# Kernel optimization log

Measured on AMD Instinct MI355X. Metric: run time of the kernel, lower is better.

## Reference

```python
import jax, jax.numpy as jnp
import numpy as np

BITS = 4
N_PACK = 32 // BITS  # int32 compression
GROUPSIZE = 128
MASK = (1 << BITS) - 1


def _unpack_int32(q, axis):
    """Unpack int32 tensor into N_PACK low-bit values along `axis`.
    Element j*N_PACK+e comes from bits [BITS*e, BITS*(e+1)) of packed word j."""
    parts = [ (q >> (BITS * e)) & MASK for e in range(N_PACK) ]
    u = jnp.stack(parts, axis=axis + 1)  # (..., P, N_PACK, ...)
    shape = list(q.shape)
    shape[axis] = shape[axis] * N_PACK
    return u.reshape(shape)


def setup_inputs() -> dict:
    key = jax.random.key(0)
    k1, k2, k3, k4, k5 = jax.random.split(key, 5)
    in_f, out_f = 4096, 12288
    tokens = 8192
    n_groups = in_f // GROUPSIZE  # 32
    x = jax.random.normal(k1, (tokens, in_f), dtype=jnp.float32)
    scales = jax.random.uniform(k2, (n_groups, out_f), dtype=jnp.float32) * 0.01 + 1e-3
    bias = jax.random.normal(k3, (out_f,), dtype=jnp.float32)
    qweight = jax.random.randint(k4, (in_f // N_PACK, out_f), jnp.iinfo(jnp.int32).min, jnp.iinfo(jnp.int32).max, dtype=jnp.int32)
    qzeros = jax.random.randint(k5, (n_groups, out_f // N_PACK), jnp.iinfo(jnp.int32).min, jnp.iinfo(jnp.int32).max, dtype=jnp.int32)
    return {"x": x, "scales": scales, "bias": bias, "qweight": qweight, "qzeros": qzeros}


def reference(x, scales, bias, qweight, qzeros):
    in_f = qweight.shape[0] * N_PACK
    out_f = qweight.shape[1]
    n_groups = scales.shape[0]
    # Unpack 4-bit weights along input-channel axis: (in_f, out_f), values 0..15
    w_int = _unpack_int32(qweight, axis=0).astype(scales.dtype)
    # Unpack zero points along output-channel axis; optimum format stores zp-1
    zp = (_unpack_int32(qzeros, axis=1) + 1).astype(scales.dtype)  # (n_groups, out_f)
    # Per-group dequant: group g covers input channels [g*GROUPSIZE, (g+1)*GROUPSIZE)
    w = (w_int.reshape(n_groups, GROUPSIZE, out_f) - zp[:, None, :]) * scales[:, None, :]
    w = w.reshape(in_f, out_f)
    # Linear: y = x @ W^T with W = w.T, i.e. x @ w
    return x @ w + bias
```

## Files before the change

kernel.cpp:

```cpp
#include <hip/hip_runtime.h>
#include <hip/hip_bf16.h>


typedef __attribute__((ext_vector_type(8))) short short8;
typedef __attribute__((ext_vector_type(4))) float f32x4;
typedef __attribute__((ext_vector_type(16))) float f32x16;

__device__ __forceinline__ short f2bf(float f) {
  unsigned u = __float_as_uint(f);
  u += 0x7fffu + ((u >> 16) & 1u);
  return (short)(u >> 16);
}

__device__ __forceinline__ void gload_lds16(const void* g, void* l) {
  __builtin_amdgcn_global_load_lds(
      (const __attribute__((address_space(1))) void*)g,
      (__attribute__((address_space(3))) void*)l,
      16, 0, 0);
}

__device__ __forceinline__ void bar() {
  asm volatile("" ::: "memory");
  __builtin_amdgcn_s_barrier();
  asm volatile("" ::: "memory");
}
__device__ __forceinline__ void wait_vm8() {
  asm volatile("s_waitcnt vmcnt(8)" ::: "memory");
}
__device__ __forceinline__ void wait_vm4() {
  asm volatile("s_waitcnt vmcnt(4)" ::: "memory");
}
__device__ __forceinline__ void wait_vm0() {
  asm volatile("s_waitcnt vmcnt(0)" ::: "memory");
}

__global__ __launch_bounds__(256) void dequant_tile_kernel(
    const int* __restrict__ qweight, const int* __restrict__ qzeros,
    const float* __restrict__ scales, short* __restrict__ Bt,
    int N, int K) {
  const int kt = K >> 5;
  const int bx = blockIdx.x;
  const int nb = bx / kt, h = bx - nb * kt;
  const int t = threadIdx.x;
  const int n = nb * 256 + t;
  const int g = h >> 2;
  const float sc = scales[(size_t)g * N + n];
  const int zw = qzeros[(size_t)g * (N >> 3) + (n >> 3)];
  const float zs = -(float)(((zw >> ((n & 7) * 4)) & 15) + 1) * sc;
  char* dst = (char*)Bt + (size_t)bx * 16384;
#pragma unroll
  for (int kw = 0; kw < 4; ++kw) {
    const int w = qweight[(size_t)(h * 4 + kw) * N + n];
    short8 v;
#pragma unroll
    for (int e = 0; e < 8; ++e)
      v[e] = f2bf(fmaf((float)((w >> (4 * e)) & 15), sc, zs));
    const int c = ((t >> 5) << 7) + ((kw >> 1) << 6) + ((kw & 1) << 5) + (t & 31);
    *(short8*)(dst + c * 16) = v;
  }
}

__global__ __launch_bounds__(256) void cvt_tile_kernel(
    const float* __restrict__ x, short* __restrict__ xb, int K) {
  const int kt = K >> 5;
  const int bx = blockIdx.x;
  const int mb = bx / kt, h = bx - mb * kt;
  const float* xs = x + (size_t)mb * 256 * K + h * 32;
  char* dst = (char*)xb + (size_t)bx * 16384;
#pragma unroll
  for (int p = 0; p < 4; ++p) {
    const int t2 = p * 256 + threadIdx.x;
    const int row = t2 >> 2, kq = t2 & 3;
    const float* s = xs + (size_t)row * K + kq * 8;
    float4 f0 = *(const float4*)s;
    float4 f1 = *(const float4*)(s + 4);
    short8 v;
    v[0] = f2bf(f0.x); v[1] = f2bf(f0.y); v[2] = f2bf(f0.z); v[3] = f2bf(f0.w);
    v[4] = f2bf(f1.x); v[5] = f2bf(f1.y); v[6] = f2bf(f1.z); v[7] = f2bf(f1.w);
    const int c = ((row >> 5) << 7) + ((kq >> 1) << 6) + ((kq & 1) << 5) + (row & 31);
    *(short8*)(dst + c * 16) = v;
  }
}

#define GBM 256
#define GBN 256

__global__ __launch_bounds__(512, 2) void gemm256_kernel(
    const short* __restrict__ At, const short* __restrict__ Bt,
    const float* __restrict__ bias, float* __restrict__ C,
    int M, int N, int K) {
  __shared__ __align__(16) char lds[4][32768];
  const int tid = threadIdx.x;
  const int nbx = N / GBN;
  const int nwg = gridDim.x;
  int bid = blockIdx.x;
  if ((nwg & 7) == 0) bid = (bid & 7) * (nwg >> 3) + (bid >> 3);
  const int mb = bid / nbx;
  const int nb = bid % nbx;
  const int bm = mb * GBM, bn = nb * GBN;

  const int wid = tid >> 6, lane = tid & 63;
  const int wr = wid >> 2, wc = wid & 3;
  const int l31 = lane & 31;
  const int lq2 = lane >> 5;

  const int P = K >> 5;

  char* lb = &lds[0][0];

  const char* aB[2];
  const char* bB[2];
  aB[0] = lb + wr * 8192 + lane * 16;
  aB[1] = aB[0] + 65536;
  bB[0] = lb + 16384 + wc * 4096 + lane * 16;
  bB[1] = bB[0] + 65536;

  const char* gA = (const char*)At + (size_t)mb * P * 16384;
  const char* gB = (const char*)Bt + (size_t)nb * P * 16384;
  char* dstA0 = lb + tid * 16;
  char* dstA1 = dstA0 + 8192;
  char* dstB0 = dstA0 + 16384;
  char* dstB1 = dstA0 + 24576;
  const size_t t16 = (size_t)tid * 16;

#define STAGE(NSL, ASRC, BSRC)                               \
  do {                                                       \
    gload_lds16((ASRC) + t16, dstA0 + (NSL) * 32768);        \
    gload_lds16((ASRC) + t16 + 8192, dstA1 + (NSL) * 32768); \
    gload_lds16((BSRC) + t16, dstB0 + (NSL) * 32768);        \
    gload_lds16((BSRC) + t16 + 8192, dstB1 + (NSL) * 32768); \
  } while (0)

  f32x16 acc[4][2] = {};

#define PHASE(SL, ST, TW)                                                     \
  do {                                                                        \
    short8 a[4][2], b[2][2];                                                  \
    _Pragma("unroll") for (int i = 0; i < 4; ++i)                             \
        _Pragma("unroll") for (int kh = 0; kh < 2; ++kh) a[i][kh] =           \
        *(const short8*)(aB[(SL) >> 1] + ((SL)&1) * 32768 + i * 2048 +        \
                         kh * 1024);                                          \
    _Pragma("unroll") for (int j = 0; j < 2; ++j)                             \
        _Pragma("unroll") for (int kh = 0; kh < 2; ++kh) b[j][kh] =           \
        *(const short8*)(bB[(SL) >> 1] + ((SL)&1) * 32768 + j * 2048 +        \
                         kh * 1024);                                          \
    if (ST) STAGE(((SL) + 3) & 3, pA + (SL) * 16384, pB + (SL) * 16384);      \
    bar();                                                                    \
    __builtin_amdgcn_s_setprio(1);                                            \
    _Pragma("unroll") for (int kh = 0; kh < 2; ++kh)                          \
        _Pragma("unroll") for (int i = 0; i < 4; ++i)                         \
        _Pragma("unroll") for (int j = 0; j < 2; ++j) acc[i][j] =             \
            __builtin_amdgcn_mfma_f32_32x32x16_bf16(a[i][kh], b[j][kh],       \
                                                    acc[i][j], 0, 0, 0);      \
    __builtin_amdgcn_s_setprio(0);                                            \
    TW;                                                                       \
    bar();                                                                    \
  } while (0)

  STAGE(0, gA, gB);
  STAGE(1, gA + 16384, gB + 16384);
  STAGE(2, gA + 32768, gB + 32768);
  wait_vm8();
  bar();

  const char* pA = gA + 3 * 16384;
  const char* pB = gB + 3 * 16384;
  const int nIt = P / 4 - 1;
  for (int it = 0; it < nIt; ++it) {
    PHASE(0, true, wait_vm8());
    PHASE(1, true, wait_vm8());
    PHASE(2, true, wait_vm8());
    PHASE(3, true, wait_vm8());
    pA += 65536;
    pB += 65536;
  }
  PHASE(0, true, wait_vm8());
  PHASE(1, false, wait_vm4());
  PHASE(2, false, wait_vm0());
  PHASE(3, false, (void)0);

#undef PHASE
#undef STAGE

  const int crow0 = bm + wr * 128 + 4 * lq2;
#pragma unroll
  for (int j = 0; j < 2; ++j) {
    const int ccol = bn + wc * 64 + j * 32 + l31;
    const float bv = bias[ccol];
#pragma unroll
    for (int i = 0; i < 4; ++i) {
#pragma unroll
      for (int reg = 0; reg < 16; ++reg) {
        const int row = crow0 + i * 32 + (reg & 3) + 8 * (reg >> 2);
        C[(size_t)row * N + ccol] = acc[i][j][reg] + bv;
      }
    }
  }
}

__global__ __launch_bounds__(256) void dequant_kernel(
    const int* __restrict__ qweight, const int* __restrict__ qzeros,
    const float* __restrict__ scales, short* __restrict__ Wt,
    int in_f, int out_f) {
  __shared__ __align__(16) short T[64][72];
  const int n0 = blockIdx.x * 64;
  const int k0 = blockIdx.y * 64;
  const int t = threadIdx.x;
  const int nl = t & 63;
  const int kw = t >> 6;
  const int n = n0 + nl;
  const int g = k0 >> 7;
  const float sc = scales[(size_t)g * out_f + n];
  const int zpw = qzeros[(size_t)g * (out_f >> 3) + (n >> 3)];
  const float zp = (float)(((zpw >> ((n & 7) * 4)) & 15) + 1);
  const float zs = zp * sc;
#pragma unroll
  for (int rr = 0; rr < 2; ++rr) {
    const int kwi = kw + rr * 4;
    const int w = qweight[(size_t)((k0 >> 3) + kwi) * out_f + n];
    short8 v;
#pragma unroll
    for (int e = 0; e < 8; ++e) {
      float f = (float)((w >> (4 * e)) & 15) * sc - zs;
      v[e] = f2bf(f);
    }
    *(short8*)&T[nl][kwi * 8] = v;
  }
  __syncthreads();
#pragma unroll
  for (int rr = 0; rr < 2; ++rr) {
    const int c = rr * 256 + t;
    const int row = c >> 3, ch = c & 7;
    *(short8*)&Wt[(size_t)(n0 + row) * in_f + k0 + ch * 8] =
        *(const short8*)&T[row][ch * 8];
  }
}

__global__ __launch_bounds__(256) void cvt_kernel(
    const float* __restrict__ x, short* __restrict__ xb, long n8) {
  long i = (long)blockIdx.x * blockDim.x + threadIdx.x;
  if (i >= n8) return;
  const float* src = x + i * 8;
  float4 a = *(const float4*)src;
  float4 b = *(const float4*)(src + 4);
  short8 v;
  v[0] = f2bf(a.x); v[1] = f2bf(a.y); v[2] = f2bf(a.z); v[3] = f2bf(a.w);
  v[4] = f2bf(b.x); v[5] = f2bf(b.y); v[6] = f2bf(b.z); v[7] = f2bf(b.w);
  *(short8*)(xb + i * 8) = v;
}

#define BM 128
#define BN 128
#define BK 64

template <bool A_BF16>
__global__ __launch_bounds__(256) void gemm_bias_kernel(
    const void* __restrict__ Av, const short* __restrict__ Bt,
    const float* __restrict__ bias, float* __restrict__ C,
    int M, int N, int K) {
  __shared__ __align__(16) short As[BM * BK];
  __shared__ __align__(16) short Bs[BN * BK];
  const int tid = threadIdx.x;
  const int bm = blockIdx.y * BM;
  const int bn = blockIdx.x * BN;
  const int wid = tid >> 6, lane = tid & 63;
  const int wr = wid >> 1, wc = wid & 1;
  const int lrow = lane & 15;
  const int lk = (lane >> 4) * 8;

  f32x4 acc[4][4] = {};

  for (int kt = 0; kt < K; kt += BK) {
    if constexpr (A_BF16) {
      const short* A = (const short*)Av;
#pragma unroll
      for (int r = 0; r < 4; ++r) {
        const int c = r * 256 + tid;
        const int row = c >> 3, ch = c & 7;
        gload_lds16(A + (size_t)(bm + row) * K + kt + ch * 8,
                    (char*)As + c * 16);
      }
    } else {
      const float* A = (const float*)Av;
#pragma unroll
      for (int r = 0; r < 4; ++r) {
        const int c = r * 256 + tid;
        const int row = c >> 3, ch = c & 7;
        const float* src = A + (size_t)(bm + row) * K + kt + ch * 8;
        float4 f0 = *(const float4*)src;
        float4 f1 = *(const float4*)(src + 4);
        short8 v;
        v[0] = f2bf(f0.x); v[1] = f2bf(f0.y); v[2] = f2bf(f0.z); v[3] = f2bf(f0.w);
        v[4] = f2bf(f1.x); v[5] = f2bf(f1.y); v[6] = f2bf(f1.z); v[7] = f2bf(f1.w);
        *(short8*)((char*)As + c * 16) = v;
      }
    }
#pragma unroll
    for (int r = 0; r < 4; ++r) {
      const int c = r * 256 + tid;
      const int row = c >> 3, ch = c & 7;
      gload_lds16(Bt + (size_t)(bn + row) * K + kt + ch * 8,
                  (char*)Bs + c * 16);
    }
    __syncthreads();
#pragma unroll
    for (int kk = 0; kk < 2; ++kk) {
      short8 af[4], bf[4];
#pragma unroll
      for (int i = 0; i < 4; ++i)
        af[i] = *(const short8*)&As[(wr * 64 + i * 16 + lrow) * BK + kk * 32 + lk];
#pragma unroll
      for (int j = 0; j < 4; ++j)
        bf[j] = *(const short8*)&Bs[(wc * 64 + j * 16 + lrow) * BK + kk * 32 + lk];
#pragma unroll
      for (int i = 0; i < 4; ++i)
#pragma unroll
        for (int j = 0; j < 4; ++j)
          acc[i][j] = __builtin_amdgcn_mfma_f32_16x16x32_bf16(
              af[i], bf[j], acc[i][j], 0, 0, 0);
    }
    __syncthreads();
  }

  const int crow0 = bm + wr * 64 + (lane >> 4) * 4;
  const int ccol0 = bn + wc * 64 + (lane & 15);
#pragma unroll
  for (int j = 0; j < 4; ++j) {
    const float bv = bias[ccol0 + j * 16];
#pragma unroll
    for (int i = 0; i < 4; ++i) {
#pragma unroll
      for (int r = 0; r < 4; ++r) {
        C[(size_t)(crow0 + i * 16 + r) * N + ccol0 + j * 16] = acc[i][j][r] + bv;
      }
    }
  }
}

__global__ __launch_bounds__(256) void naive_kernel(
    const float* __restrict__ x, const float* __restrict__ scales,
    const float* __restrict__ bias, const int* __restrict__ qw,
    const int* __restrict__ qz, float* __restrict__ out,
    int M, int K, int N) {
  long idx = (long)blockIdx.x * blockDim.x + threadIdx.x;
  if (idx >= (long)M * N) return;
  const int n = (int)(idx % N);
  const int m = (int)(idx / N);
  float acc = 0.f;
  for (int g = 0; g < K / 128; ++g) {
    const float sc = scales[(size_t)g * N + n];
    const float zp =
        (float)(((qz[(size_t)g * (N >> 3) + (n >> 3)] >> ((n & 7) * 4)) & 15) + 1);
    const float zs = zp * sc;
    for (int kw = 0; kw < 16; ++kw) {
      const int w = qw[(size_t)(g * 16 + kw) * N + n];
      const float* xp = &x[(size_t)m * K + g * 128 + kw * 8];
#pragma unroll
      for (int e = 0; e < 8; ++e)
        acc += xp[e] * ((float)((w >> (4 * e)) & 15) * sc - zs);
    }
  }
  out[idx] = acc + bias[n];
}

extern "C" void kernel_launch(void* const* d_in, const int* in_sizes, int n_in,
                              void* d_out, int out_size, void* d_ws,
                              size_t ws_size, hipStream_t stream) {
  const float* x = (const float*)d_in[0];
  const float* scales = (const float*)d_in[1];
  const float* bias = (const float*)d_in[2];
  const int* qweight = (const int*)d_in[3];
  const int* qzeros = (const int*)d_in[4];
  float* out = (float*)d_out;

  const int out_f = in_sizes[2];
  const int kwords = in_sizes[3] / out_f;
  const int in_f = kwords * 8;
  const int tokens = in_sizes[0] / in_f;
  const int M = tokens, K = in_f, N = out_f;

  const size_t wt_bytes = (size_t)K * N * sizeof(short);
  const size_t xb_bytes = (size_t)M * K * sizeof(short);

  const bool div128 = (M % BM == 0) && (N % BN == 0) && (K % BK == 0) &&
                      (K % 128 == 0) && (N % 64 == 0);
  const bool div256 = (M % GBM == 0) && (N % GBN == 0) && (K % 256 == 0);

  if (div256 && ws_size >= wt_bytes + xb_bytes) {
    short* Btile = (short*)d_ws;
    short* Atile = (short*)((char*)d_ws + wt_bytes);
    const int kt = K >> 5;
    dequant_tile_kernel<<<(N / 256) * kt, 256, 0, stream>>>(
        qweight, qzeros, scales, Btile, N, K);
    cvt_tile_kernel<<<(M / 256) * kt, 256, 0, stream>>>(x, Atile, K);
    gemm256_kernel<<<(M / GBM) * (N / GBN), 512, 0, stream>>>(
        Atile, Btile, bias, out, M, N, K);
  } else if (div128 && ws_size >= wt_bytes + xb_bytes) {
    short* Wt = (short*)d_ws;
    short* xb = (short*)((char*)d_ws + wt_bytes);
    dequant_kernel<<<dim3(N / 64, K / 64), 256, 0, stream>>>(
        qweight, qzeros, scales, Wt, K, N);
    const long n8 = (long)M * K / 8;
    cvt_kernel<<<(int)((n8 + 255) / 256), 256, 0, stream>>>(x, xb, n8);
    gemm_bias_kernel<true><<<dim3(N / BN, M / BM), 256, 0, stream>>>(
        xb, Wt, bias, out, M, N, K);
  } else if (div128 && ws_size >= wt_bytes) {
    short* Wt = (short*)d_ws;
    dequant_kernel<<<dim3(N / 64, K / 64), 256, 0, stream>>>(
        qweight, qzeros, scales, Wt, K, N);
    gemm_bias_kernel<false><<<dim3(N / BN, M / BM), 256, 0, stream>>>(
        x, Wt, bias, out, M, N, K);
  } else {
    const long total = (long)M * N;
    naive_kernel<<<(int)((total + 255) / 256), 256, 0, stream>>>(
        x, scales, bias, qweight, qzeros, out, M, K, N);
  }
}
```

Measured before the change: 820.7 us.

## Restructure GEMM main loop into double-buffered 64-wide K phases with one barrier

Replaces the 4-slot ring with one K-slice per phase by phases that each consume two LDS slices (64 K-elements), staging the next two slices at once. Each phase now needs a single barrier and a full vmcnt(0) wait instead of two barriers with partial waits. This halves barrier count per K step but reduces prefetch depth: loads must complete within one phase instead of overlapping across several.

Result: slower. 850.6 us (+3.6%).

```diff
diff --git a/kernel.cpp b/kernel.cpp
--- a/kernel.cpp
+++ b/kernel.cpp
@@ -23,12 +23,6 @@
   asm volatile("" ::: "memory");
   __builtin_amdgcn_s_barrier();
   asm volatile("" ::: "memory");
-}
-__device__ __forceinline__ void wait_vm8() {
-  asm volatile("s_waitcnt vmcnt(8)" ::: "memory");
-}
-__device__ __forceinline__ void wait_vm4() {
-  asm volatile("s_waitcnt vmcnt(4)" ::: "memory");
 }
 __device__ __forceinline__ void wait_vm0() {
   asm volatile("s_waitcnt vmcnt(0)" ::: "memory");
@@ -105,6 +99,7 @@
   const int lq2 = lane >> 5;
 
   const int P = K >> 5;
+  const int NP = P >> 1;
 
   char* lb = &lds[0][0];
 
@@ -131,55 +126,67 @@
     gload_lds16((BSRC) + t16 + 8192, dstB1 + (NSL) * 32768); \
   } while (0)
 
-  f32x16 acc[4][2] = {};
-
-#define PHASE(SL, ST, TW)                                                     \
+#define RDFRAG(SL, A, B)                                                      \
   do {                                                                        \
-    short8 a[4][2], b[2][2];                                                  \
     _Pragma("unroll") for (int i = 0; i < 4; ++i)                             \
-        _Pragma("unroll") for (int kh = 0; kh < 2; ++kh) a[i][kh] =           \
+        _Pragma("unroll") for (int kh = 0; kh < 2; ++kh) A[i][kh] =           \
         *(const short8*)(aB[(SL) >> 1] + ((SL)&1) * 32768 + i * 2048 +        \
                          kh * 1024);                                          \
     _Pragma("unroll") for (int j = 0; j < 2; ++j)                             \
-        _Pragma("unroll") for (int kh = 0; kh < 2; ++kh) b[j][kh] =           \
+        _Pragma("unroll") for (int kh = 0; kh < 2; ++kh) B[j][kh] =           \
         *(const short8*)(bB[(SL) >> 1] + ((SL)&1) * 32768 + j * 2048 +        \
                          kh * 1024);                                          \
-    if (ST) STAGE(((SL) + 3) & 3, pA + (SL) * 16384, pB + (SL) * 16384);      \
-    bar();                                                                    \
+  } while (0)
+
+  f32x16 acc[4][2] = {};
+
+#define MFMA16(A, B)                                                          \
+  do {                                                                        \
     __builtin_amdgcn_s_setprio(1);                                            \
     _Pragma("unroll") for (int kh = 0; kh < 2; ++kh)                          \
         _Pragma("unroll") for (int i = 0; i < 4; ++i)                         \
         _Pragma("unroll") for (int j = 0; j < 2; ++j) acc[i][j] =             \
-            __builtin_amdgcn_mfma_f32_32x32x16_bf16(a[i][kh], b[j][kh],       \
+            __builtin_amdgcn_mfma_f32_32x32x16_bf16(A[i][kh], B[j][kh],       \
                                                     acc[i][j], 0, 0, 0);      \
     __builtin_amdgcn_s_setprio(0);                                            \
-    TW;                                                                       \
+  } while (0)
+
+#define PHASE64(S0, S1, T0, T1, O0, O1, ST)                                   \
+  do {                                                                        \
+    short8 a0[4][2], b0[2][2];                                                \
+    RDFRAG(S0, a0, b0);                                                       \
+    if (ST) {                                                                 \
+      STAGE(T0, pA + (O0) * 16384, pB + (O0) * 16384);                        \
+      STAGE(T1, pA + (O1) * 16384, pB + (O1) * 16384);                        \
+    }                                                                         \
+    MFMA16(a0, b0);                                                           \
+    short8 a1[4][2], b1[2][2];                                                \
+    RDFRAG(S1, a1, b1);                                                       \
+    MFMA16(a1, b1);                                                           \
+    if (ST) { wait_vm0(); }                                                   \
     bar();                                                                    \
   } while (0)
 
   STAGE(0, gA, gB);
   STAGE(1, gA + 16384, gB + 16384);
-  STAGE(2, gA + 32768, gB + 32768);
-  wait_vm8();
+  wait_vm0();
   bar();
 
-  const char* pA = gA + 3 * 16384;
-  const char* pB = gB + 3 * 16384;
-  const int nIt = P / 4 - 1;
+  const char* pA = gA;
+  const char* pB = gB;
+  const int nIt = NP / 2 - 1;
   for (int it = 0; it < nIt; ++it) {
-    PHASE(0, true, wait_vm8());
-    PHASE(1, true, wait_vm8());
-    PHASE(2, true, wait_vm8());
-    PHASE(3, true, wait_vm8());
+    PHASE64(0, 1, 2, 3, 2, 3, true);
+    PHASE64(2, 3, 0, 1, 4, 5, true);
     pA += 65536;
     pB += 65536;
   }
-  PHASE(0, true, wait_vm8());
-  PHASE(1, false, wait_vm4());
-  PHASE(2, false, wait_vm0());
-  PHASE(3, false, (void)0);
-
-#undef PHASE
+  PHASE64(0, 1, 2, 3, 2, 3, true);
+  PHASE64(2, 3, 0, 1, 4, 5, false);
+
+#undef PHASE64
+#undef MFMA16
+#undef RDFRAG
 #undef STAGE
 
   const int crow0 = bm + wr * 128 + 4 * lq2;
```
